# Kernel optimization log

Measured on AMD Instinct MI355X. Metric: run time of the kernel, lower is better.

The kernel has to match this reference:

```python
import jax, jax.numpy as jnp
import numpy as np

N_NODES = 50000
N_EDGES = 800000
IN_C = 16
HID_C = 16
OUT_C = 10
N_GRAPHS = 500
EDGE_DIM = 3
MLP_HID = 25
BN_EPS = 1e-5


def setup_inputs() -> dict:
    key = jax.random.key(0)
    ks = iter(jax.random.split(key, 40))

    def nrm(shape, scale=1.0):
        return jax.random.normal(next(ks), shape, dtype=jnp.float32) * scale

    inp = {}
    inp["x"] = nrm((N_NODES, IN_C))
    inp["edge_index"] = jax.random.randint(next(ks), (2, N_EDGES), 0, N_NODES, dtype=jnp.int32)
    inp["edge_attr"] = jax.random.uniform(next(ks), (N_EDGES, EDGE_DIM), dtype=jnp.float32)
    inp["batch"] = jnp.sort(jax.random.randint(next(ks), (N_NODES,), 0, N_GRAPHS, dtype=jnp.int32))

    def bn_params():
        g = jax.random.uniform(next(ks), (MLP_HID,), minval=0.8, maxval=1.2, dtype=jnp.float32)
        b = nrm((MLP_HID,), 0.1)
        mu = nrm((MLP_HID,), 0.1)
        var = jax.random.uniform(next(ks), (MLP_HID,), minval=0.5, maxval=1.5, dtype=jnp.float32)
        return g, b, mu, var

    # edge MLP 1: 3 -> 25 -> IN_C*HID_C
    inp["W1a"] = nrm((EDGE_DIM, MLP_HID), 0.3)
    inp["b1a"] = nrm((MLP_HID,), 0.05)
    inp["g1"], inp["bt1"], inp["m1"], inp["v1"] = bn_params()
    inp["W1b"] = nrm((MLP_HID, IN_C * HID_C), 0.1)
    inp["b1b"] = nrm((IN_C * HID_C,), 0.05)
    inp["root1"] = nrm((IN_C, HID_C), 0.2)
    inp["bias1"] = nrm((HID_C,), 0.05)

    # edge MLP 2: 3 -> 25 -> HID_C*HID_C
    inp["W2a"] = nrm((EDGE_DIM, MLP_HID), 0.3)
    inp["b2a"] = nrm((MLP_HID,), 0.05)
    inp["g2"], inp["bt2"], inp["m2"], inp["v2"] = bn_params()
    inp["W2b"] = nrm((MLP_HID, HID_C * HID_C), 0.1)
    inp["b2b"] = nrm((HID_C * HID_C,), 0.05)
    inp["root2"] = nrm((HID_C, HID_C), 0.2)
    inp["bias2"] = nrm((HID_C,), 0.05)

    # final MLP([HID_C, OUT_C]) -> single plain linear (plain_last)
    inp["fcW"] = nrm((HID_C, OUT_C), 0.2)
    inp["fcb"] = nrm((OUT_C,), 0.05)
    return inp


def _edge_mlp(e, Wa, ba, g, bt, mu, var, Wb, bb):
    # Linear -> BatchNorm(eval) -> ReLU -> (dropout=eval identity) -> Linear
    h = e @ Wa + ba
    h = g * (h - mu) * jax.lax.rsqrt(var + BN_EPS) + bt
    h = jax.nn.relu(h)
    return h @ Wb + bb


def _nnconv(x, src, dst, w_edge, root, bias, out_dim):
    # message: x_j [E,in] times per-edge weight [E,in,out]
    msg = jnp.einsum("ei,eio->eo", x[src], w_edge)
    agg = jax.ops.segment_sum(msg, dst, num_segments=N_NODES)
    deg = jax.ops.segment_sum(jnp.ones((src.shape[0],), msg.dtype), dst, num_segments=N_NODES)
    agg = agg / jnp.maximum(deg, 1.0)[:, None]  # mean aggregation
    return agg + x @ root + bias


def reference(x, edge_index, edge_attr, batch,
              W1a, b1a, g1, bt1, m1, v1, W1b, b1b, root1, bias1,
              W2a, b2a, g2, bt2, m2, v2, W2b, b2b, root2, bias2,
              fcW, fcb):
    src, dst = edge_index[0], edge_index[1]

    w1 = _edge_mlp(edge_attr, W1a, b1a, g1, bt1, m1, v1, W1b, b1b).reshape(-1, IN_C, HID_C)
    x = jax.nn.elu(_nnconv(x, src, dst, w1, root1, bias1, HID_C))

    w2 = _edge_mlp(edge_attr, W2a, b2a, g2, bt2, m2, v2, W2b, b2b).reshape(-1, HID_C, HID_C)
    x = jax.nn.elu(_nnconv(x, src, dst, w2, root2, bias2, HID_C))

    # global mean pooling over graphs
    pooled = jax.ops.segment_sum(x, batch, num_segments=N_GRAPHS)
    cnt = jax.ops.segment_sum(jnp.ones((x.shape[0],), x.dtype), batch, num_segments=N_GRAPHS)
    pooled = pooled / jnp.maximum(cnt, 1.0)[:, None]

    return pooled @ fcW + fcb  # [N_GRAPHS, OUT_C]
```

## Files before the change

### kernel.cpp

```cpp
#include <hip/hip_runtime.h>
#include <math.h>

#define N_NODES 50000
#define N_EDGES 800000
#define IN_C 16
#define HID_C 16
#define OUT_C 10
#define N_GRAPHS 500
#define EDGE_DIM 3
#define MLP_HID 25
#define BN_EPS 1e-5f

#define SCAN_NB ((N_NODES + 255) / 256)

typedef __attribute__((ext_vector_type(8))) _Float16 half8;
typedef __attribute__((ext_vector_type(2))) _Float16 half2v;
typedef __attribute__((ext_vector_type(4))) float f32x4;
union U4H8 { uint4 u; half8 h; half2v p[4]; };
union HU { _Float16 h; unsigned short u; };


__global__ __launch_bounds__(256) void setup_kernel(
    const float* __restrict__ W1a, const float* __restrict__ b1a,
    const float* __restrict__ g1, const float* __restrict__ bt1,
    const float* __restrict__ m1, const float* __restrict__ v1,
    const float* __restrict__ W2a, const float* __restrict__ b2a,
    const float* __restrict__ g2, const float* __restrict__ bt2,
    const float* __restrict__ m2, const float* __restrict__ v2,
    const float* __restrict__ W1b, const float* __restrict__ b1b,
    const float* __restrict__ W2b, const float* __restrict__ b2b,
    const int* __restrict__ batch,
    float* __restrict__ AC1, float* __restrict__ AC2,
    unsigned int* __restrict__ WF1, unsigned int* __restrict__ WF2,
    int* __restrict__ goff, int* __restrict__ cnt, int* __restrict__ ticket)
{
    const int blk = blockIdx.x;
    const int tid = threadIdx.x;
    if (blk < 7) {
        int t = blk * 256 + tid;
        if (t >= 1664) return;
        const float *Wb, *bb; unsigned int *WH;
        int tl = t;
        if (t < 832) { Wb = W1b; bb = b1b; WH = WF1; }
        else { tl = t - 832; Wb = W2b; bb = b2b; WH = WF2; }
        int m = tl >> 6;
        int L = tl & 63;
        int q = L >> 4, o = L & 15;
        unsigned int hi[8];
        for (int j = 0; j < 8; ++j) {
            int kp = m*32 + q*8 + j;
            int k = kp >> 4, i = kp & 15;
            float w = (k < 25) ? Wb[k*256 + i*16 + o] : bb[i*16 + o];
            HU cv; cv.h = (_Float16)w;
            hi[j] = cv.u;
        }
        int base = (m*64 + L) * 4;
        for (int d = 0; d < 4; ++d)
            WH[base + d] = hi[2*d] | (hi[2*d+1] << 16);
        return;
    }
    if (blk == 7 || blk == 8) {
        if (blk == 7) {
            if (tid < 26) {
                int k = tid;
                if (k < 25) {
                    float sc = g1[k] / sqrtf(v1[k] + BN_EPS);
                    AC1[k*4+0] = sc * W1a[0*MLP_HID+k];
                    AC1[k*4+1] = sc * W1a[1*MLP_HID+k];
                    AC1[k*4+2] = sc * W1a[2*MLP_HID+k];
                    AC1[k*4+3] = sc * (b1a[k] - m1[k]) + bt1[k];
                } else {
                    AC1[100] = 0.f; AC1[101] = 0.f; AC1[102] = 0.f; AC1[103] = 1.f;
                }
            } else if (tid >= 32 && tid < 58) {
                int k = tid - 32;
                if (k < 25) {
                    float sc = g2[k] / sqrtf(v2[k] + BN_EPS);
                    AC2[k*4+0] = sc * W2a[0*MLP_HID+k];
                    AC2[k*4+1] = sc * W2a[1*MLP_HID+k];
                    AC2[k*4+2] = sc * W2a[2*MLP_HID+k];
                    AC2[k*4+3] = sc * (b2a[k] - m2[k]) + bt2[k];
                } else {
                    AC2[100] = 0.f; AC2[101] = 0.f; AC2[102] = 0.f; AC2[103] = 1.f;
                }
            }
        }
        int g = (blk - 7) * 256 + tid;
        if (g <= N_GRAPHS) {
            int lo = 0, hi = N_NODES;
            while (lo < hi) {
                int mid = (lo + hi) >> 1;
                if (batch[mid] < g) lo = mid + 1; else hi = mid;
            }
            goff[g] = lo;
        }
        return;
    }
    int idx = (blk - 9) * 256 + tid;
    if (idx < N_NODES) cnt[idx] = 0;
    if (blk == 9 && tid == 0) *ticket = 0;
}


__global__ __launch_bounds__(256) void rank_kernel(const int* __restrict__ dst,
                                                   int* __restrict__ cnt,
                                                   int* __restrict__ rank) {
    int e = blockIdx.x * blockDim.x + threadIdx.x;
    if (e < N_EDGES) rank[e] = atomicAdd(&cnt[dst[e]], 1);
}

__global__ __launch_bounds__(256) void scan_p1(const int* __restrict__ cnt,
                                               int* __restrict__ bsum,
                                               int* __restrict__ bpre,
                                               int* __restrict__ off,
                                               int* __restrict__ ticket) {
    __shared__ int lds[256];
    __shared__ int sDone;
    int t = threadIdx.x;
    int idx = blockIdx.x * 256 + t;
    lds[t] = (idx < N_NODES) ? cnt[idx] : 0;
    __syncthreads();
    for (int d = 128; d > 0; d >>= 1) {
        if (t < d) lds[t] += lds[t + d];
        __syncthreads();
    }
    if (t == 0) {
        bsum[blockIdx.x] = lds[0];
        __threadfence();
        sDone = atomicAdd(ticket, 1);
    }
    __syncthreads();
    if (sDone != SCAN_NB - 1) return;
    __threadfence();
    int v = (t < SCAN_NB) ? bsum[t] : 0;
    __syncthreads();
    lds[t] = v;
    __syncthreads();
    for (int d = 1; d < 256; d <<= 1) {
        int u = (t >= d) ? lds[t - d] : 0;
        __syncthreads();
        lds[t] += u;
        __syncthreads();
    }
    if (t < SCAN_NB) bpre[t] = (t > 0) ? lds[t - 1] : 0;
    if (t == 255) off[N_NODES] = lds[255];
}

__global__ __launch_bounds__(256) void scan_p3(const int* __restrict__ cnt,
                                               const int* __restrict__ bpre,
                                               int* __restrict__ off) {
    __shared__ int lds[256];
    int t = threadIdx.x;
    int idx = blockIdx.x * 256 + t;
    int v = (idx < N_NODES) ? cnt[idx] : 0;
    lds[t] = v;
    __syncthreads();
    for (int d = 1; d < 256; d <<= 1) {
        int u = (t >= d) ? lds[t - d] : 0;
        __syncthreads();
        lds[t] += u;
        __syncthreads();
    }
    if (idx < N_NODES) off[idx] = bpre[blockIdx.x] + lds[t] - v;
}


__global__ __launch_bounds__(256) void edge_mfma6_kernel(
    const float* __restrict__ xin,
    const int* __restrict__ src,
    const int* __restrict__ dst,
    const int* __restrict__ rank,
    const int* __restrict__ off,
    const float* __restrict__ eattr,
    const float* __restrict__ AC,
    const unsigned int* __restrict__ WF,
    float* __restrict__ msg_buf)
{
    __shared__ uint4 wf_s[832];
    const int tid = threadIdx.x;
    #pragma unroll
    for (int it = 0; it < 4; ++it) {
        int gi = tid + it*256;
        if (gi < 832) wf_s[gi] = ((const uint4*)WF)[gi];
    }
    __syncthreads();

    const int wave = tid >> 6;
    const int lane = tid & 63;
    const int q    = lane >> 4;
    const int el   = lane & 15;
    const int i0   = (q & 1) * 8;
    const bool bsel = (q >> 1) != 0;
    const int E0   = (blockIdx.x * 4 + wave) * 64;

    const int sAll = src[E0 + lane];
    const int dAll = dst[E0 + lane];
    const int rAll = rank[E0 + lane];
    const int pAll = off[dAll] + rAll;

    int   sT[4];
    float a0[4], a1[4], a2[4];
    #pragma unroll
    for (int t = 0; t < 4; ++t) {
        sT[t] = __shfl(sAll, t*16 + el);
        int e = E0 + t*16 + el;
        a0[t] = eattr[(size_t)e*3+0];
        a1[t] = eattr[(size_t)e*3+1];
        a2[t] = eattr[(size_t)e*3+2];
    }

    U4H8 xf[4];
    #pragma unroll
    for (int t = 0; t < 4; ++t) {
        const float4* xp = (const float4*)(xin + (size_t)sT[t]*16 + i0);
        const float4 xl = xp[0], xh = xp[1];
        const float x8[8] = {xl.x,xl.y,xl.z,xl.w,xh.x,xh.y,xh.z,xh.w};
        #pragma unroll
        for (int j = 0; j < 4; ++j) {
            half2v tv; tv.x = (_Float16)x8[2*j]; tv.y = (_Float16)x8[2*j+1];
            xf[t].p[j] = tv;
        }
    }

    f32x4 acc0 = {0.f,0.f,0.f,0.f}, acc1 = {0.f,0.f,0.f,0.f};
    f32x4 acc2 = {0.f,0.f,0.f,0.f}, acc3 = {0.f,0.f,0.f,0.f};
    #pragma unroll 1
    for (int m = 0; m < 13; ++m) {
        const float4 Ae = *(const float4*)(AC + m*8);
        const float4 Ao = *(const float4*)(AC + m*8 + 4);
        const float A0 = bsel ? Ao.x : Ae.x;
        const float A1 = bsel ? Ao.y : Ae.y;
        const float A2 = bsel ? Ao.z : Ae.z;
        const float A3 = bsel ? Ao.w : Ae.w;
        U4H8 w; w.u = wf_s[m*64 + lane];
        #pragma unroll
        for (int t = 0; t < 4; ++t) {
            float h = fmaxf(fmaf(a2[t], A2, fmaf(a1[t], A1,
                              fmaf(a0[t], A0, A3))), 0.f);
            _Float16 hh = (_Float16)h;
            half2v h2; h2.x = hh; h2.y = hh;
            U4H8 f;
            #pragma unroll
            for (int j = 0; j < 4; ++j) f.p[j] = h2 * xf[t].p[j];
            f32x4 a = (t==0) ? acc0 : (t==1) ? acc1 : (t==2) ? acc2 : acc3;
            a = __builtin_amdgcn_mfma_f32_16x16x32_f16(w.h, f.h, a, 0, 0, 0);
            if (t==0) acc0 = a; else if (t==1) acc1 = a;
            else if (t==2) acc2 = a; else acc3 = a;
        }
    }

    #pragma unroll
    for (int t = 0; t < 4; ++t) {
        int row = __shfl(pAll, t*16 + el);
        f32x4 a = (t==0) ? acc0 : (t==1) ? acc1 : (t==2) ? acc2 : acc3;
        *(f32x4*)(msg_buf + (size_t)row * HID_C + q*4) = a;
    }
}

__global__ __launch_bounds__(256) void node_gather_kernel(
    const float* __restrict__ xin, const float* __restrict__ msg_buf,
    const int* __restrict__ off,
    const float* __restrict__ root, const float* __restrict__ bias,
    float* __restrict__ xout)
{
    int t = blockIdx.x * blockDim.x + threadIdx.x;
    int n = t >> 4;
    int o = t & 15;
    if (n >= N_NODES) return;
    int lo = off[n], hi = off[n+1];
    float inv = 1.f / fmaxf((float)(hi - lo), 1.f);

    float s0 = 0.f, s1 = 0.f, s2 = 0.f, s3 = 0.f;
    int r = lo;
    for (; r + 4 <= hi; r += 4) {
        s0 += msg_buf[(size_t)r     * HID_C + o];
        s1 += msg_buf[(size_t)(r+1) * HID_C + o];
        s2 += msg_buf[(size_t)(r+2) * HID_C + o];
        s3 += msg_buf[(size_t)(r+3) * HID_C + o];
    }
    for (; r < hi; ++r) s0 += msg_buf[(size_t)r * HID_C + o];
    float s = (s0 + s1) + (s2 + s3);

    float acc = fmaf(s, inv, bias[o]);
    const float* xr = xin + (size_t)n * IN_C;
    #pragma unroll
    for (int i = 0; i < IN_C; ++i)
        acc = fmaf(xr[i], root[i*HID_C+o], acc);
    xout[(size_t)n*HID_C + o] = acc > 0.f ? acc : (expf(acc) - 1.f);
}

__global__ __launch_bounds__(64) void pool_final_kernel(
    const float* __restrict__ xin, const int* __restrict__ goff,
    const float* __restrict__ fcW, const float* __restrict__ fcb,
    float* __restrict__ out)
{
    __shared__ float part[4][HID_C];
    __shared__ float pooled[HID_C];
    int g = blockIdx.x;
    int t = threadIdx.x;
    int c = t & 15, sub = t >> 4;
    int lo = goff[g], hi = goff[g+1];
    float s = 0.f;
    for (int n = lo + sub; n < hi; n += 4)
        s += xin[(size_t)n*HID_C + c];
    part[sub][c] = s;
    __syncthreads();
    if (t < HID_C) {
        pooled[t] = (part[0][t] + part[1][t] + part[2][t] + part[3][t])
                    / fmaxf((float)(hi - lo), 1.f);
    }
    __syncthreads();
    if (t < OUT_C) {
        float acc = fcb[t];
        #pragma unroll
        for (int i = 0; i < HID_C; ++i)
            acc = fmaf(pooled[i], fcW[i*OUT_C+t], acc);
        out[g*OUT_C + t] = acc;
    }
}


extern "C" void kernel_launch(void* const* d_in, const int* in_sizes, int n_in,
                              void* d_out, int out_size, void* d_ws, size_t ws_size,
                              hipStream_t stream)
{
    const float* x     = (const float*)d_in[0];
    const int*   ei    = (const int*)d_in[1];
    const float* eattr = (const float*)d_in[2];
    const int*   batch = (const int*)d_in[3];
    const float* W1a   = (const float*)d_in[4];
    const float* b1a   = (const float*)d_in[5];
    const float* g1    = (const float*)d_in[6];
    const float* bt1   = (const float*)d_in[7];
    const float* m1    = (const float*)d_in[8];
    const float* v1    = (const float*)d_in[9];
    const float* W1b   = (const float*)d_in[10];
    const float* b1b   = (const float*)d_in[11];
    const float* root1 = (const float*)d_in[12];
    const float* bias1 = (const float*)d_in[13];
    const float* W2a   = (const float*)d_in[14];
    const float* b2a   = (const float*)d_in[15];
    const float* g2    = (const float*)d_in[16];
    const float* bt2   = (const float*)d_in[17];
    const float* m2    = (const float*)d_in[18];
    const float* v2    = (const float*)d_in[19];
    const float* W2b   = (const float*)d_in[20];
    const float* b2b   = (const float*)d_in[21];
    const float* root2 = (const float*)d_in[22];
    const float* bias2 = (const float*)d_in[23];
    const float* fcW   = (const float*)d_in[24];
    const float* fcb   = (const float*)d_in[25];

    const int* src = ei;
    const int* dst = ei + N_EDGES;

    float* ws   = (float*)d_ws;
    float* MSG  = ws;
    float* X1   = ws + 12800000;
    float* X2   = ws + 13600000;
    int*   RANK = (int*)(ws + 14400000);
    int*   CNT  = (int*)(ws + 15200000);
    int*   OFF  = (int*)(ws + 15250000);
    int*   GOFF = (int*)(ws + 15300064);
    unsigned int* WF1 = (unsigned int*)(ws + 15300576);
    unsigned int* WF2 = (unsigned int*)(ws + 15303904);
    float* AC1  = ws + 15307232;
    float* AC2  = ws + 15307344;
    int*   BSUM = (int*)(ws + 15307456);
    int*   BPRE = (int*)(ws + 15307712);
    int*   TICK = (int*)(ws + 15307968);

    setup_kernel<<<9 + SCAN_NB, 256, 0, stream>>>(
        W1a, b1a, g1, bt1, m1, v1, W2a, b2a, g2, bt2, m2, v2,
        W1b, b1b, W2b, b2b, batch, AC1, AC2, WF1, WF2, GOFF, CNT, TICK);
    rank_kernel<<<N_EDGES/256, 256, 0, stream>>>(dst, CNT, RANK);
    scan_p1<<<SCAN_NB, 256, 0, stream>>>(CNT, BSUM, BPRE, OFF, TICK);
    scan_p3<<<SCAN_NB, 256, 0, stream>>>(CNT, BPRE, OFF);

    edge_mfma6_kernel<<<N_EDGES/256, 256, 0, stream>>>(x, src, dst, RANK, OFF,
                                                       eattr, AC1, WF1, MSG);
    node_gather_kernel<<<(N_NODES*16+255)/256, 256, 0, stream>>>(x, MSG, OFF,
                                                                 root1, bias1, X1);

    edge_mfma6_kernel<<<N_EDGES/256, 256, 0, stream>>>(X1, src, dst, RANK, OFF,
                                                       eattr, AC2, WF2, MSG);
    node_gather_kernel<<<(N_NODES*16+255)/256, 256, 0, stream>>>(X1, MSG, OFF,
                                                                 root2, bias2, X2);

    pool_final_kernel<<<N_GRAPHS, 64, 0, stream>>>(X2, GOFF, fcW, fcb, (float*)d_out);
}
```

Baseline: 261.0 us.

## Fuse edge messages with segmented in-wave reduction and atomics, drop message buffer

Edges are permuted once into destination-sorted order, with source, destination and padded edge attributes stored contiguously. The edge kernel then reduces MFMA outputs for runs of equal destination using wave shuffles and adds each run's partial sum into a node aggregate with float atomics. The per-node gather then becomes a simple finalize that reads one aggregate row. This removes the large per-edge message buffer write and read in both layers. The cost is an extra permute pass, atomic traffic, zeroing of the aggregate buffers in setup, and a summation order that is no longer deterministic.

```diff
diff --git a/kernel.cpp b/kernel.cpp
--- a/kernel.cpp
+++ b/kernel.cpp
@@ -12,6 +12,8 @@
 #define BN_EPS 1e-5f
 
 #define SCAN_NB ((N_NODES + 255) / 256)
+#define NZB 200
+#define ZERO_F4 412500
 
 typedef __attribute__((ext_vector_type(8))) _Float16 half8;
 typedef __attribute__((ext_vector_type(2))) _Float16 half2v;
@@ -32,7 +34,7 @@
     const int* __restrict__ batch,
     float* __restrict__ AC1, float* __restrict__ AC2,
     unsigned int* __restrict__ WF1, unsigned int* __restrict__ WF2,
-    int* __restrict__ goff, int* __restrict__ cnt, int* __restrict__ ticket)
+    int* __restrict__ goff, float* __restrict__ zbase, int* __restrict__ ticket)
 {
     const int blk = blockIdx.x;
     const int tid = threadIdx.x;
@@ -96,8 +98,10 @@
         }
         return;
     }
-    int idx = (blk - 9) * 256 + tid;
-    if (idx < N_NODES) cnt[idx] = 0;
+    int z = (blk - 9) * 256 + tid;
+    f32x4* Z = (f32x4*)zbase;
+    const f32x4 zero4 = {0.f, 0.f, 0.f, 0.f};
+    for (int i = z; i < ZERO_F4; i += NZB * 256) Z[i] = zero4;
     if (blk == 9 && tid == 0) *ticket = 0;
 }
 
@@ -164,17 +168,34 @@
     if (idx < N_NODES) off[idx] = bpre[blockIdx.x] + lds[t] - v;
 }
 
-
-__global__ __launch_bounds__(256) void edge_mfma6_kernel(
+__global__ __launch_bounds__(256) void permute_kernel(
+    const int* __restrict__ src, const int* __restrict__ dst,
+    const int* __restrict__ rank, const int* __restrict__ off,
+    const float* __restrict__ eattr,
+    int* __restrict__ ssrc, int* __restrict__ ddst, float4* __restrict__ ea4)
+{
+    int e = blockIdx.x * blockDim.x + threadIdx.x;
+    int d = dst[e];
+    int p = off[d] + rank[e];
+    ssrc[p] = src[e];
+    ddst[p] = d;
+    float4 a;
+    a.x = eattr[(size_t)e*3+0];
+    a.y = eattr[(size_t)e*3+1];
+    a.z = eattr[(size_t)e*3+2];
+    a.w = 0.f;
+    ea4[p] = a;
+}
+
+
+__global__ __launch_bounds__(256) void edge_fused_kernel(
     const float* __restrict__ xin,
-    const int* __restrict__ src,
-    const int* __restrict__ dst,
-    const int* __restrict__ rank,
-    const int* __restrict__ off,
-    const float* __restrict__ eattr,
+    const int* __restrict__ ssrc,
+    const int* __restrict__ ddst,
+    const float4* __restrict__ ea4,
     const float* __restrict__ AC,
     const unsigned int* __restrict__ WF,
-    float* __restrict__ msg_buf)
+    float* __restrict__ AGG)
 {
     __shared__ uint4 wf_s[832];
     const int tid = threadIdx.x;
@@ -191,22 +212,18 @@
     const int el   = lane & 15;
     const int i0   = (q & 1) * 8;
     const bool bsel = (q >> 1) != 0;
-    const int E0   = (blockIdx.x * 4 + wave) * 64;
-
-    const int sAll = src[E0 + lane];
-    const int dAll = dst[E0 + lane];
-    const int rAll = rank[E0 + lane];
-    const int pAll = off[dAll] + rAll;
+    const int P0   = (blockIdx.x * 4 + wave) * 64;
+
+    const int sAll = ssrc[P0 + lane];
+    const int nAll = ddst[P0 + lane];
 
     int   sT[4];
     float a0[4], a1[4], a2[4];
     #pragma unroll
     for (int t = 0; t < 4; ++t) {
         sT[t] = __shfl(sAll, t*16 + el);
-        int e = E0 + t*16 + el;
-        a0[t] = eattr[(size_t)e*3+0];
-        a1[t] = eattr[(size_t)e*3+1];
-        a2[t] = eattr[(size_t)e*3+2];
+        float4 at = ea4[P0 + t*16 + el];
+        a0[t] = at.x; a1[t] = at.y; a2[t] = at.z;
     }
 
     U4H8 xf[4];
@@ -251,15 +268,33 @@
 
     #pragma unroll
     for (int t = 0; t < 4; ++t) {
-        int row = __shfl(pAll, t*16 + el);
         f32x4 a = (t==0) ? acc0 : (t==1) ? acc1 : (t==2) ? acc2 : acc3;
-        *(f32x4*)(msg_buf + (size_t)row * HID_C + q*4) = a;
-    }
-}
-
-__global__ __launch_bounds__(256) void node_gather_kernel(
-    const float* __restrict__ xin, const float* __restrict__ msg_buf,
-    const int* __restrict__ off,
+        const int nt = __shfl(nAll, t*16 + el);
+        #pragma unroll
+        for (int s = 1; s < 16; s <<= 1) {
+            float ux = __shfl(a.x, lane - s);
+            float uy = __shfl(a.y, lane - s);
+            float uz = __shfl(a.z, lane - s);
+            float uw = __shfl(a.w, lane - s);
+            int   ku = __shfl(nt,  lane - s);
+            if (el >= s && ku == nt) {
+                a.x += ux; a.y += uy; a.z += uz; a.w += uw;
+            }
+        }
+        int nn = __shfl(nAll, t*16 + el + 1);
+        if (el == 15 || nn != nt) {
+            float* p = AGG + (size_t)nt * HID_C + q*4;
+            unsafeAtomicAdd(p+0, a.x);
+            unsafeAtomicAdd(p+1, a.y);
+            unsafeAtomicAdd(p+2, a.z);
+            unsafeAtomicAdd(p+3, a.w);
+        }
+    }
+}
+
+__global__ __launch_bounds__(256) void node_finalize_kernel(
+    const float* __restrict__ xin, const float* __restrict__ AGG,
+    const int* __restrict__ cnt,
     const float* __restrict__ root, const float* __restrict__ bias,
     float* __restrict__ xout)
 {
@@ -267,26 +302,13 @@
     int n = t >> 4;
     int o = t & 15;
     if (n >= N_NODES) return;
-    int lo = off[n], hi = off[n+1];
-    float inv = 1.f / fmaxf((float)(hi - lo), 1.f);
-
-    float s0 = 0.f, s1 = 0.f, s2 = 0.f, s3 = 0.f;
-    int r = lo;
-    for (; r + 4 <= hi; r += 4) {
-        s0 += msg_buf[(size_t)r     * HID_C + o];
-        s1 += msg_buf[(size_t)(r+1) * HID_C + o];
-        s2 += msg_buf[(size_t)(r+2) * HID_C + o];
-        s3 += msg_buf[(size_t)(r+3) * HID_C + o];
-    }
-    for (; r < hi; ++r) s0 += msg_buf[(size_t)r * HID_C + o];
-    float s = (s0 + s1) + (s2 + s3);
-
-    float acc = fmaf(s, inv, bias[o]);
+    float inv = 1.f / fmaxf((float)cnt[n], 1.f);
+    float acc = fmaf(AGG[t], inv, bias[o]);
     const float* xr = xin + (size_t)n * IN_C;
     #pragma unroll
     for (int i = 0; i < IN_C; ++i)
         acc = fmaf(xr[i], root[i*HID_C+o], acc);
-    xout[(size_t)n*HID_C + o] = acc > 0.f ? acc : (expf(acc) - 1.f);
+    xout[t] = acc > 0.f ? acc : (expf(acc) - 1.f);
 }
 
 __global__ __launch_bounds__(64) void pool_final_kernel(
@@ -355,37 +377,45 @@
     const int* dst = ei + N_EDGES;
 
     float* ws   = (float*)d_ws;
-    float* MSG  = ws;
-    float* X1   = ws + 12800000;
-    float* X2   = ws + 13600000;
-    int*   RANK = (int*)(ws + 14400000);
-    int*   CNT  = (int*)(ws + 15200000);
-    int*   OFF  = (int*)(ws + 15250000);
-    int*   GOFF = (int*)(ws + 15300064);
-    unsigned int* WF1 = (unsigned int*)(ws + 15300576);
-    unsigned int* WF2 = (unsigned int*)(ws + 15303904);
-    float* AC1  = ws + 15307232;
-    float* AC2  = ws + 15307344;
-    int*   BSUM = (int*)(ws + 15307456);
-    int*   BPRE = (int*)(ws + 15307712);
-    int*   TICK = (int*)(ws + 15307968);
-
-    setup_kernel<<<9 + SCAN_NB, 256, 0, stream>>>(
+    int*   SSRC = (int*)(ws + 0);
+    int*   DDST = (int*)(ws + 800000);
+    float* EA4  = ws + 1600000;
+    float* AGG1 = ws + 4800000;
+    float* AGG2 = ws + 5600000;
+    int*   CNT  = (int*)(ws + 6400000);
+    int*   RANK = (int*)(ws + 6450000);
+    int*   OFF  = (int*)(ws + 7250000);
+    int*   GOFF = (int*)(ws + 7300064);
+    unsigned int* WF1 = (unsigned int*)(ws + 7300576);
+    unsigned int* WF2 = (unsigned int*)(ws + 7303904);
+    float* AC1  = ws + 7307232;
+    float* AC2  = ws + 7307344;
+    int*   BSUM = (int*)(ws + 7307456);
+    int*   BPRE = (int*)(ws + 7307712);
+    int*   TICK = (int*)(ws + 7307968);
+    float* X1   = ws + 7308032;
+    float* X2   = ws + 8108032;
+
+    setup_kernel<<<9 + NZB, 256, 0, stream>>>(
         W1a, b1a, g1, bt1, m1, v1, W2a, b2a, g2, bt2, m2, v2,
-        W1b, b1b, W2b, b2b, batch, AC1, AC2, WF1, WF2, GOFF, CNT, TICK);
+        W1b, b1b, W2b, b2b, batch, AC1, AC2, WF1, WF2, GOFF, AGG1, TICK);
     rank_kernel<<<N_EDGES/256, 256, 0, stream>>>(dst, CNT, RANK);
     scan_p1<<<SCAN_NB, 256, 0, stream>>>(CNT, BSUM, BPRE, OFF, TICK);
     scan_p3<<<SCAN_NB, 256, 0, stream>>>(CNT, BPRE, OFF);
-
-    edge_mfma6_kernel<<<N_EDGES/256, 256, 0, stream>>>(x, src, dst, RANK, OFF,
-                                                       eattr, AC1, WF1, MSG);
-    node_gather_kernel<<<(N_NODES*16+255)/256, 256, 0, stream>>>(x, MSG, OFF,
-                                                                 root1, bias1, X1);
-
-    edge_mfma6_kernel<<<N_EDGES/256, 256, 0, stream>>>(X1, src, dst, RANK, OFF,
-                                                       eattr, AC2, WF2, MSG);
-    node_gather_kernel<<<(N_NODES*16+255)/256, 256, 0, stream>>>(X1, MSG, OFF,
-                                                                 root2, bias2, X2);
+    permute_kernel<<<N_EDGES/256, 256, 0, stream>>>(src, dst, RANK, OFF, eattr,
+                                                    SSRC, DDST, (float4*)EA4);
+
+    edge_fused_kernel<<<N_EDGES/256, 256, 0, stream>>>(x, SSRC, DDST,
+                                                       (const float4*)EA4,
+                                                       AC1, WF1, AGG1);
+    node_finalize_kernel<<<(N_NODES*16)/256, 256, 0, stream>>>(x, AGG1, CNT,
+                                                               root1, bias1, X1);
+
+    edge_fused_kernel<<<N_EDGES/256, 256, 0, stream>>>(X1, SSRC, DDST,
+                                                       (const float4*)EA4,
+                                                       AC2, WF2, AGG2);
+    node_finalize_kernel<<<(N_NODES*16)/256, 256, 0, stream>>>(X1, AGG2, CNT,
+                                                               root2, bias2, X2);
 
     pool_final_kernel<<<N_GRAPHS, 64, 0, stream>>>(X2, GOFF, fcW, fcb, (float*)d_out);
 }
```

After: 281.8 us. 1.08x slower.

## Pre-pack edge attrs to float4, store node features as fp16, vectorize node gather

Applied to the files above, without the earlier changes.

The setup kernel now pads edge attributes to float4 and converts the input features to packed fp16. The node gather kernel writes an fp16 copy of its output for the next layer, so the edge MFMA kernel gathers 32 bytes per source row instead of 64 and skips the per-edge conversion. The node gather is rewritten to use four threads per node with float4 message loads and the root matrix held in shared memory. In exchange there is an extra pre-pass writing 12.8MB of float4 edge attributes plus an extra fp16 feature write.

```diff
diff --git a/kernel.cpp b/kernel.cpp
--- a/kernel.cpp
+++ b/kernel.cpp
@@ -12,6 +12,7 @@
 #define BN_EPS 1e-5f
 
 #define SCAN_NB ((N_NODES + 255) / 256)
+#define NZB 200
 
 typedef __attribute__((ext_vector_type(8))) _Float16 half8;
 typedef __attribute__((ext_vector_type(2))) _Float16 half2v;
@@ -30,9 +31,12 @@
     const float* __restrict__ W1b, const float* __restrict__ b1b,
     const float* __restrict__ W2b, const float* __restrict__ b2b,
     const int* __restrict__ batch,
+    const float* __restrict__ xin, const float* __restrict__ eattr,
     float* __restrict__ AC1, float* __restrict__ AC2,
     unsigned int* __restrict__ WF1, unsigned int* __restrict__ WF2,
-    int* __restrict__ goff, int* __restrict__ cnt, int* __restrict__ ticket)
+    int* __restrict__ goff, int* __restrict__ cnt,
+    float4* __restrict__ ea4, unsigned int* __restrict__ xh0,
+    int* __restrict__ ticket)
 {
     const int blk = blockIdx.x;
     const int tid = threadIdx.x;
@@ -96,8 +100,26 @@
         }
         return;
     }
-    int idx = (blk - 9) * 256 + tid;
-    if (idx < N_NODES) cnt[idx] = 0;
+    const int bt = (blk - 9) * 256 + tid;
+    const int STR = NZB * 256;
+    int4* c4 = (int4*)cnt;
+    const int4 z4 = {0, 0, 0, 0};
+    for (int i = bt; i < 12500; i += STR) c4[i] = z4;
+    for (int e = bt; e < N_EDGES; e += STR) {
+        float4 a;
+        a.x = eattr[e*3+0];
+        a.y = eattr[e*3+1];
+        a.z = eattr[e*3+2];
+        a.w = 0.f;
+        ea4[e] = a;
+    }
+    const float2* x2 = (const float2*)xin;
+    for (int i = bt; i < 400000; i += STR) {
+        float2 v = x2[i];
+        HU h0; h0.h = (_Float16)v.x;
+        HU h1; h1.h = (_Float16)v.y;
+        xh0[i] = (unsigned int)h0.u | ((unsigned int)h1.u << 16);
+    }
     if (blk == 9 && tid == 0) *ticket = 0;
 }
 
@@ -165,13 +187,13 @@
 }
 
 
-__global__ __launch_bounds__(256) void edge_mfma6_kernel(
-    const float* __restrict__ xin,
+__global__ __launch_bounds__(256) void edge_mfma7_kernel(
+    const unsigned short* __restrict__ xh,
     const int* __restrict__ src,
     const int* __restrict__ dst,
     const int* __restrict__ rank,
     const int* __restrict__ off,
-    const float* __restrict__ eattr,
+    const float4* __restrict__ ea4,
     const float* __restrict__ AC,
     const unsigned int* __restrict__ WF,
     float* __restrict__ msg_buf)
@@ -203,24 +225,14 @@
     #pragma unroll
     for (int t = 0; t < 4; ++t) {
         sT[t] = __shfl(sAll, t*16 + el);
-        int e = E0 + t*16 + el;
-        a0[t] = eattr[(size_t)e*3+0];
-        a1[t] = eattr[(size_t)e*3+1];
-        a2[t] = eattr[(size_t)e*3+2];
+        float4 at = ea4[E0 + t*16 + el];
+        a0[t] = at.x; a1[t] = at.y; a2[t] = at.z;
     }
 
     U4H8 xf[4];
     #pragma unroll
-    for (int t = 0; t < 4; ++t) {
-        const float4* xp = (const float4*)(xin + (size_t)sT[t]*16 + i0);
-        const float4 xl = xp[0], xh = xp[1];
-        const float x8[8] = {xl.x,xl.y,xl.z,xl.w,xh.x,xh.y,xh.z,xh.w};
-        #pragma unroll
-        for (int j = 0; j < 4; ++j) {
-            half2v tv; tv.x = (_Float16)x8[2*j]; tv.y = (_Float16)x8[2*j+1];
-            xf[t].p[j] = tv;
-        }
-    }
+    for (int t = 0; t < 4; ++t)
+        xf[t].u = *(const uint4*)(const void*)(xh + (size_t)sT[t]*16 + i0);
 
     f32x4 acc0 = {0.f,0.f,0.f,0.f}, acc1 = {0.f,0.f,0.f,0.f};
     f32x4 acc2 = {0.f,0.f,0.f,0.f}, acc3 = {0.f,0.f,0.f,0.f};
@@ -261,32 +273,68 @@
     const float* __restrict__ xin, const float* __restrict__ msg_buf,
     const int* __restrict__ off,
     const float* __restrict__ root, const float* __restrict__ bias,
-    float* __restrict__ xout)
+    float* __restrict__ xout, unsigned int* __restrict__ xh_out)
 {
+    __shared__ float root_s[IN_C * HID_C];
+    if (threadIdx.x < 64)
+        ((float4*)root_s)[threadIdx.x] = ((const float4*)root)[threadIdx.x];
+    __syncthreads();
+
     int t = blockIdx.x * blockDim.x + threadIdx.x;
-    int n = t >> 4;
-    int o = t & 15;
+    int n = t >> 2;
     if (n >= N_NODES) return;
+    int c0 = (t & 3) * 4;
     int lo = off[n], hi = off[n+1];
     float inv = 1.f / fmaxf((float)(hi - lo), 1.f);
 
-    float s0 = 0.f, s1 = 0.f, s2 = 0.f, s3 = 0.f;
+    const f32x4* m4 = (const f32x4*)msg_buf;
+    const int qi = c0 >> 2;
+    f32x4 s0 = {0.f,0.f,0.f,0.f}, s1 = {0.f,0.f,0.f,0.f};
     int r = lo;
-    for (; r + 4 <= hi; r += 4) {
-        s0 += msg_buf[(size_t)r     * HID_C + o];
-        s1 += msg_buf[(size_t)(r+1) * HID_C + o];
-        s2 += msg_buf[(size_t)(r+2) * HID_C + o];
-        s3 += msg_buf[(size_t)(r+3) * HID_C + o];
-    }
-    for (; r < hi; ++r) s0 += msg_buf[(size_t)r * HID_C + o];
-    float s = (s0 + s1) + (s2 + s3);
-
-    float acc = fmaf(s, inv, bias[o]);
-    const float* xr = xin + (size_t)n * IN_C;
+    for (; r + 2 <= hi; r += 2) {
+        s0 += m4[(size_t)r*4 + qi];
+        s1 += m4[(size_t)(r+1)*4 + qi];
+    }
+    if (r < hi) s0 += m4[(size_t)r*4 + qi];
+    f32x4 s = s0 + s1;
+
+    const float4 bv = *(const float4*)(bias + c0);
+    f32x4 acc;
+    acc.x = fmaf(s.x, inv, bv.x);
+    acc.y = fmaf(s.y, inv, bv.y);
+    acc.z = fmaf(s.z, inv, bv.z);
+    acc.w = fmaf(s.w, inv, bv.w);
+
+    const float4* x4 = (const float4*)(xin + (size_t)n * IN_C);
     #pragma unroll
-    for (int i = 0; i < IN_C; ++i)
-        acc = fmaf(xr[i], root[i*HID_C+o], acc);
-    xout[(size_t)n*HID_C + o] = acc > 0.f ? acc : (expf(acc) - 1.f);
+    for (int j = 0; j < 4; ++j) {
+        float4 xv = x4[j];
+        #pragma unroll
+        for (int k = 0; k < 4; ++k) {
+            float xi = (k==0) ? xv.x : (k==1) ? xv.y : (k==2) ? xv.z : xv.w;
+            const float4 rv = *(const float4*)(root_s + (j*4+k)*HID_C + c0);
+            acc.x = fmaf(xi, rv.x, acc.x);
+            acc.y = fmaf(xi, rv.y, acc.y);
+            acc.z = fmaf(xi, rv.z, acc.z);
+            acc.w = fmaf(xi, rv.w, acc.w);
+        }
+    }
+
+    acc.x = acc.x > 0.f ? acc.x : (expf(acc.x) - 1.f);
+    acc.y = acc.y > 0.f ? acc.y : (expf(acc.y) - 1.f);
+    acc.z = acc.z > 0.f ? acc.z : (expf(acc.z) - 1.f);
+    acc.w = acc.w > 0.f ? acc.w : (expf(acc.w) - 1.f);
+    *(f32x4*)(xout + (size_t)n * HID_C + c0) = acc;
+
+    if (xh_out) {
+        HU h0, h1, h2, h3;
+        h0.h = (_Float16)acc.x; h1.h = (_Float16)acc.y;
+        h2.h = (_Float16)acc.z; h3.h = (_Float16)acc.w;
+        uint2 pk;
+        pk.x = (unsigned int)h0.u | ((unsigned int)h1.u << 16);
+        pk.y = (unsigned int)h2.u | ((unsigned int)h3.u << 16);
+        ((uint2*)xh_out)[n*4 + qi] = pk;
+    }
 }
 
 __global__ __launch_bounds__(64) void pool_final_kernel(
@@ -369,23 +417,29 @@
     int*   BSUM = (int*)(ws + 15307456);
     int*   BPRE = (int*)(ws + 15307712);
     int*   TICK = (int*)(ws + 15307968);
-
-    setup_kernel<<<9 + SCAN_NB, 256, 0, stream>>>(
+    float* EA4  = ws + 15308032;
+    unsigned int* XH0 = (unsigned int*)(ws + 18508032);
+    unsigned int* XH1 = (unsigned int*)(ws + 18908032);
+
+    setup_kernel<<<9 + NZB, 256, 0, stream>>>(
         W1a, b1a, g1, bt1, m1, v1, W2a, b2a, g2, bt2, m2, v2,
-        W1b, b1b, W2b, b2b, batch, AC1, AC2, WF1, WF2, GOFF, CNT, TICK);
+        W1b, b1b, W2b, b2b, batch, x, eattr,
+        AC1, AC2, WF1, WF2, GOFF, CNT, (float4*)EA4, XH0, TICK);
     rank_kernel<<<N_EDGES/256, 256, 0, stream>>>(dst, CNT, RANK);
     scan_p1<<<SCAN_NB, 256, 0, stream>>>(CNT, BSUM, BPRE, OFF, TICK);
     scan_p3<<<SCAN_NB, 256, 0, stream>>>(CNT, BPRE, OFF);
 
-    edge_mfma6_kernel<<<N_EDGES/256, 256, 0, stream>>>(x, src, dst, RANK, OFF,
-                                                       eattr, AC1, WF1, MSG);
-    node_gather_kernel<<<(N_NODES*16+255)/256, 256, 0, stream>>>(x, MSG, OFF,
-                                                                 root1, bias1, X1);
-
-    edge_mfma6_kernel<<<N_EDGES/256, 256, 0, stream>>>(X1, src, dst, RANK, OFF,
-                                                       eattr, AC2, WF2, MSG);
-    node_gather_kernel<<<(N_NODES*16+255)/256, 256, 0, stream>>>(X1, MSG, OFF,
-                                                                 root2, bias2, X2);
+    edge_mfma7_kernel<<<N_EDGES/256, 256, 0, stream>>>(
+        (const unsigned short*)XH0, src, dst, RANK, OFF,
+        (const float4*)EA4, AC1, WF1, MSG);
+    node_gather_kernel<<<(N_NODES*4 + 255)/256, 256, 0, stream>>>(
+        x, MSG, OFF, root1, bias1, X1, XH1);
+
+    edge_mfma7_kernel<<<N_EDGES/256, 256, 0, stream>>>(
+        (const unsigned short*)XH1, src, dst, RANK, OFF,
+        (const float4*)EA4, AC2, WF2, MSG);
+    node_gather_kernel<<<(N_NODES*4 + 255)/256, 256, 0, stream>>>(
+        X1, MSG, OFF, root2, bias2, X2, (unsigned int*)nullptr);
 
     pool_final_kernel<<<N_GRAPHS, 64, 0, stream>>>(X2, GOFF, fcW, fcb, (float*)d_out);
 }
```

Result: faster. 251.4 us (-3.6%).
